# Optimization experiments

Measured on AMD Instinct MI355X. Metric: run time of the kernel, lower is better.

Reference implementation:

```python
import jax, jax.numpy as jnp
import numpy as np

N0, D, H, E0 = 50000, 128, 128, 800000
N1, E1, A, B, C = 20000, 320000, 100000, 64, 10


def _gcn(x, row, col, ew, n, W, b):
    # GCNConv: out = D^-1/2 (A + I) D^-1/2 (x W) + b, with edge weights
    xw = x @ W
    sl = jnp.arange(n)
    r = jnp.concatenate([row, sl])
    c = jnp.concatenate([col, sl])
    w = jnp.concatenate([ew, jnp.ones((n,), ew.dtype)])
    deg = jax.ops.segment_sum(w, c, num_segments=n)
    dinv = jax.lax.rsqrt(jnp.maximum(deg, 1e-12))
    norm = dinv[r] * w * dinv[c]
    return jax.ops.segment_sum(norm[:, None] * xw[r], c, num_segments=n) + b


def _block(x, row, col, ew, n, W1, b1, W2, b2, Wl, bl):
    # Block with num_inner_layers=2, jumping_knowledge='cat'
    x1 = jax.nn.relu(_gcn(x, row, col, ew, n, W1, b1))
    x2 = jax.nn.relu(_gcn(x1, row, col, ew, n, W2, b2))
    return jnp.concatenate([x1, x2], axis=1) @ Wl + bl


def _seg_max(x, idx, n):
    m = jax.ops.segment_max(x, idx, num_segments=n)
    return jnp.where(jnp.isfinite(m), m, 0.0)  # empty segments -> 0 like scatter_max default


def _lin_init(k, i, o):
    s = 1.0 / np.sqrt(i)
    return jax.random.uniform(k, (i, o), jnp.float32, -s, s)


def setup_inputs() -> dict:
    key = jax.random.key(0)
    ks = jax.random.split(key, 20)
    x = jax.random.normal(ks[0], (N0, D), jnp.float32)
    edge_index0 = jax.random.randint(ks[1], (2, E0), 0, N0)
    edge_weight0 = jax.random.uniform(ks[2], (E0,), jnp.float32)
    batch0 = jnp.sort(jax.random.randint(ks[3], (N0,), 0, B))
    cover_row = jax.random.randint(ks[4], (A,), 0, N0)
    cover_col = jnp.concatenate([jnp.arange(N1), jax.random.randint(ks[5], (A - N1,), 0, N1)])
    edge_index1 = jax.random.randint(ks[6], (2, E1), 0, N1)
    edge_weight1 = jax.random.uniform(ks[7], (E1,), jnp.float32)
    batch1 = jnp.sort(jax.random.randint(ks[8], (N1,), 0, B))
    params = dict(
        w_in1=_lin_init(ks[9], D, H), b_in1=jnp.zeros((H,), jnp.float32),
        w_in2=_lin_init(ks[10], H, H), b_in2=jnp.zeros((H,), jnp.float32),
        w_in_lin=_lin_init(ks[11], 2 * H, H), b_in_lin=jnp.zeros((H,), jnp.float32),
        w_b1=_lin_init(ks[12], 2 * H, H), b_b1=jnp.zeros((H,), jnp.float32),
        w_b2=_lin_init(ks[13], H, H), b_b2=jnp.zeros((H,), jnp.float32),
        w_b_lin=_lin_init(ks[14], 2 * H, H), b_b_lin=jnp.zeros((H,), jnp.float32),
        bn_gamma=jnp.ones((4 * H,), jnp.float32), bn_beta=jnp.zeros((4 * H,), jnp.float32),
        w_l1=_lin_init(ks[15], 4 * H, H), b_l1=jnp.zeros((H,), jnp.float32),
        w_l2=_lin_init(ks[16], H, C), b_l2=jnp.zeros((C,), jnp.float32),
    )
    return dict(x=x, edge_index0=edge_index0, edge_weight0=edge_weight0, batch0=batch0,
                cover_row=cover_row, cover_col=cover_col, edge_index1=edge_index1,
                edge_weight1=edge_weight1, batch1=batch1, **params)


def reference(x, edge_index0, edge_weight0, batch0, cover_row, cover_col,
              edge_index1, edge_weight1, batch1,
              w_in1, b_in1, w_in2, b_in2, w_in_lin, b_in_lin,
              w_b1, b_b1, w_b2, b_b2, w_b_lin, b_b_lin,
              bn_gamma, bn_beta, w_l1, b_l1, w_l2, b_l2):
    r0, c0 = edge_index0[0], edge_index0[1]
    h = jax.nn.relu(_block(x, r0, c0, edge_weight0, N0, w_in1, b_in1, w_in2, b_in2, w_in_lin, b_in_lin))
    xs = [jax.ops.segment_sum(h, batch0, num_segments=B), _seg_max(h, batch0, B)]
    # cover_pool_node: add + max over k-plex cover assignments
    hg = h[cover_row]
    h2 = jnp.concatenate([jax.ops.segment_sum(hg, cover_col, num_segments=N1),
                          _seg_max(hg, cover_col, N1)], axis=1)
    r1, c1 = edge_index1[0], edge_index1[1]
    h2 = jax.nn.relu(_block(h2, r1, c1, edge_weight1, N1, w_b1, b_b1, w_b2, b_b2, w_b_lin, b_b_lin))
    xs.append(jax.ops.segment_sum(h2, batch1, num_segments=B))
    xs.append(_seg_max(h2, batch1, B))
    z = jnp.concatenate(xs, axis=1)  # [B, 4H]
    # BatchNorm1d in eval mode: running stats (mean=0, var=1), eps=1e-5
    z = z * (bn_gamma * jax.lax.rsqrt(jnp.asarray(1.0 + 1e-5, z.dtype))) + bn_beta
    z = jax.nn.relu(z @ w_l1 + b_l1)
    logits = z @ w_l2 + b_l2  # dropout skipped (eval mode)
    return jax.nn.softmax(logits, axis=-1)
```

## Files before the change

### kernel.cpp

```cpp
#include <hip/hip_runtime.h>
#include <cmath>

#define HF 128
#define EPB 2048

namespace {

typedef __attribute__((ext_vector_type(8))) short short8;
typedef __attribute__((ext_vector_type(4))) float f32x4;

inline int cdiv(int a, int b) { return (a + b - 1) / b; }

__device__ inline unsigned short f2bf(float x) {
    unsigned u = __float_as_uint(x);
    return (unsigned short)((u + 0x7fffu + ((u >> 16) & 1u)) >> 16);
}
__device__ inline float bf2f(unsigned short u) {
    return __uint_as_float((unsigned)u << 16);
}
__device__ inline float bflo(unsigned v) { return __uint_as_float(v << 16); }
__device__ inline float bfhi(unsigned v) { return __uint_as_float(v & 0xffff0000u); }

#define FIXS 4194304.0f
#define FIXINV 2.384185791015625e-07f
#define SUMMASK ((1ULL << 40) - 1)

template <int K, bool AF32>
__device__ __forceinline__ void gemm_dev(int bid, const void* __restrict__ A1v, int lda1,
                                         const void* __restrict__ A2v, int lda2,
                                         const unsigned short* __restrict__ wpk,
                                         const float* __restrict__ bias, int relu,
                                         unsigned short* __restrict__ out, int N) {
    const int t = threadIdx.x;
    const int wv = t >> 6, lane = t & 63;
    const int l15 = lane & 15, lhi = lane >> 4;
    const int rbase = bid * 128 + wv * 32;

    f32x4 acc[2][8];
#pragma unroll
    for (int i = 0; i < 2; ++i)
#pragma unroll
        for (int g = 0; g < 8; ++g) acc[i][g] = {0.f, 0.f, 0.f, 0.f};

    int r[2];
#pragma unroll
    for (int ri = 0; ri < 2; ++ri) {
        int rr = rbase + ri * 16 + l15;
        r[ri] = (rr < N) ? rr : (N - 1);
    }

    for (int kc = 0; kc < K / 32; ++kc) {
        int kb = kc * 32 + lhi * 8;
        short8 a[2];
#pragma unroll
        for (int ri = 0; ri < 2; ++ri) {
            if (AF32) {
                const float* A = (const float*)A1v;
                const float* p = A + (size_t)r[ri] * lda1 + kb;
                float4 f0 = *reinterpret_cast<const float4*>(p);
                float4 f1 = *reinterpret_cast<const float4*>(p + 4);
                a[ri][0] = (short)f2bf(f0.x); a[ri][1] = (short)f2bf(f0.y);
                a[ri][2] = (short)f2bf(f0.z); a[ri][3] = (short)f2bf(f0.w);
                a[ri][4] = (short)f2bf(f1.x); a[ri][5] = (short)f2bf(f1.y);
                a[ri][6] = (short)f2bf(f1.z); a[ri][7] = (short)f2bf(f1.w);
            } else {
                const unsigned short* base;
                int kk, ld;
                if (K == 256 && kb >= 128) { base = (const unsigned short*)A2v; kk = kb - 128; ld = lda2; }
                else                       { base = (const unsigned short*)A1v; kk = kb;       ld = lda1; }
                a[ri] = *reinterpret_cast<const short8*>(base + (size_t)r[ri] * ld + kk);
            }
        }
        const unsigned short* wb = wpk + (size_t)(kc * 8) * 512 + lane * 8;
#pragma unroll
        for (int g = 0; g < 8; ++g) {
            short8 b = *reinterpret_cast<const short8*>(wb + (size_t)g * 512);
            acc[0][g] = __builtin_amdgcn_mfma_f32_16x16x32_bf16(a[0], b, acc[0][g], 0, 0, 0);
            acc[1][g] = __builtin_amdgcn_mfma_f32_16x16x32_bf16(a[1], b, acc[1][g], 0, 0, 0);
        }
    }

#pragma unroll
    for (int ri = 0; ri < 2; ++ri) {
#pragma unroll
        for (int g = 0; g < 8; ++g) {
            int col = l15 + g * 16;
            float bb = bias ? bias[col] : 0.f;
#pragma unroll
            for (int e = 0; e < 4; ++e) {
                int rr = rbase + ri * 16 + lhi * 4 + e;
                if (rr < N) {
                    float v = acc[ri][g][e] + bb;
                    if (relu) v = fmaxf(v, 0.f);
                    out[(size_t)rr * 128 + col] = f2bf(v);
                }
            }
        }
    }
}

template <int K, bool AF32>
__global__ void k_mfma_gemm(const void* __restrict__ A1v, int lda1,
                            const void* __restrict__ A2v, int lda2,
                            const unsigned short* __restrict__ wpk,
                            const float* __restrict__ bias, int relu,
                            unsigned short* __restrict__ out, int N) {
    gemm_dev<K, AF32>(blockIdx.x, A1v, lda1, A2v, lda2, wpk, bias, relu, out, N);
}

__device__ __forceinline__ void hist_dev(int e, int E, const int* __restrict__ col,
                                         const float* __restrict__ ew,
                                         unsigned long long* __restrict__ dc,
                                         unsigned* __restrict__ rank) {
    if (e < E) {
        unsigned long long v = (1ULL << 40) | (unsigned long long)(ew[e] * FIXS + 0.5f);
        unsigned long long old = atomicAdd(&dc[col[e]], v);
        rank[e] = (unsigned)(old >> 40);
    }
}

__device__ inline void scan256(int* s, int v, int gid, int n, int* __restrict__ excl,
                               int* __restrict__ partial, int pb) {
    s[threadIdx.x] = v;
    __syncthreads();
    for (int off = 1; off < 256; off <<= 1) {
        int t = (threadIdx.x >= off) ? s[threadIdx.x - off] : 0;
        __syncthreads();
        s[threadIdx.x] += t;
        __syncthreads();
    }
    if (gid < n) excl[gid] = s[threadIdx.x] - v;
    if (threadIdx.x == 255) partial[pb] = s[255];
}

__device__ __forceinline__ void fill_dev(int b, int t, const int* __restrict__ row,
                                         const int* __restrict__ col, const float* __restrict__ ew,
                                         const unsigned* __restrict__ rank,
                                         const float* __restrict__ dinv, const int* __restrict__ rp,
                                         int2* __restrict__ ed, int E, int Nn) {
    int xcd = b & 7, chunk = b >> 3;
    int lo = (int)((long long)Nn * xcd >> 3), hi = (int)((long long)Nn * (xcd + 1) >> 3);
    int base = chunk * EPB;
#pragma unroll
    for (int i = 0; i < EPB; i += 256) {
        int e = base + i + t;
        if (e < E) {
            int c = col[e];
            if (c >= lo && c < hi) {
                int r = row[e];
                ed[rp[c] + rank[e]] = make_int2(r, __float_as_int(ew[e] * dinv[r] * dinv[c]));
            }
        }
    }
}

__device__ __forceinline__ void gather_dev(int b, const unsigned* __restrict__ xw, int n,
                                           const int* __restrict__ rp, const int2* __restrict__ ed,
                                           const float* __restrict__ dinv,
                                           const float* __restrict__ bias,
                                           unsigned* __restrict__ out) {
    int wid = (b * 256 + (int)threadIdx.x) >> 6;
    if (wid >= n) return;
    int lane = threadIdx.x & 63;
    int s = rp[wid], e = rp[wid + 1];
    float d = dinv[wid];
    unsigned v = xw[(size_t)wid * 64 + lane];
    float ax = bflo(v) * d * d, ay = bfhi(v) * d * d;
    float bx = 0.f, by = 0.f, cx = 0.f, cy = 0.f, dx = 0.f, dy = 0.f;
    int i = s;
    for (; i + 4 <= e; i += 4) {
        unsigned long long p0 = __builtin_nontemporal_load((const unsigned long long*)(ed + i));
        unsigned long long p1 = __builtin_nontemporal_load((const unsigned long long*)(ed + i + 1));
        unsigned long long p2 = __builtin_nontemporal_load((const unsigned long long*)(ed + i + 2));
        unsigned long long p3 = __builtin_nontemporal_load((const unsigned long long*)(ed + i + 3));
        unsigned v0 = xw[(size_t)(unsigned)(p0 & 0xffffffffu) * 64 + lane];
        unsigned v1 = xw[(size_t)(unsigned)(p1 & 0xffffffffu) * 64 + lane];
        unsigned v2 = xw[(size_t)(unsigned)(p2 & 0xffffffffu) * 64 + lane];
        unsigned v3 = xw[(size_t)(unsigned)(p3 & 0xffffffffu) * 64 + lane];
        float c0 = __uint_as_float((unsigned)(p0 >> 32));
        float c1 = __uint_as_float((unsigned)(p1 >> 32));
        float c2 = __uint_as_float((unsigned)(p2 >> 32));
        float c3 = __uint_as_float((unsigned)(p3 >> 32));
        ax += c0 * bflo(v0); ay += c0 * bfhi(v0);
        bx += c1 * bflo(v1); by += c1 * bfhi(v1);
        cx += c2 * bflo(v2); cy += c2 * bfhi(v2);
        dx += c3 * bflo(v3); dy += c3 * bfhi(v3);
    }
    for (; i < e; ++i) {
        unsigned long long p0 = __builtin_nontemporal_load((const unsigned long long*)(ed + i));
        unsigned v0 = xw[(size_t)(unsigned)(p0 & 0xffffffffu) * 64 + lane];
        float c0 = __uint_as_float((unsigned)(p0 >> 32));
        ax += c0 * bflo(v0); ay += c0 * bfhi(v0);
    }
    ax += bx + cx + dx;
    ay += by + cy + dy;
    float2 bb = *reinterpret_cast<const float2*>(bias + lane * 2);
    ax = fmaxf(ax + bb.x, 0.f);
    ay = fmaxf(ay + bb.y, 0.f);
    out[(size_t)wid * 64 + lane] = (unsigned)f2bf(ax) | ((unsigned)f2bf(ay) << 16);
}

__global__ void k_prep0(const float* __restrict__ w0, const float* __restrict__ w1,
                        const float* __restrict__ w2, const float* __restrict__ w3,
                        const float* __restrict__ w4, const float* __restrict__ w5,
                        unsigned short* __restrict__ wpk,
                        const int* __restrict__ b0, int n0, const int* __restrict__ b1,
                        int n1, int B, int* __restrict__ bst0, int* __restrict__ bst1) {
    int b = blockIdx.x, t = threadIdx.x;
    if (b < 576) {
        int idx = b * 256 + t;
        const float* src; int local;
        if      (idx < 16384)  { src = w0; local = idx; }
        else if (idx < 32768)  { src = w1; local = idx - 16384; }
        else if (idx < 65536)  { src = w2; local = idx - 32768; }
        else if (idx < 98304)  { src = w3; local = idx - 65536; }
        else if (idx < 114688) { src = w4; local = idx - 98304; }
        else                   { src = w5; local = idx - 114688; }
        int e = local & 7, lane = (local >> 3) & 63, g = (local >> 9) & 7, kc = local >> 12;
        int colw = (lane & 15) + 16 * g;
        int k = kc * 32 + ((lane >> 4) << 3) + e;
        wpk[idx] = f2bf(src[k * 128 + colw]);
        return;
    }
    int idx = t;
    if (idx < 2 * (B + 1)) {
        int which = idx > B;
        int bb = which ? idx - (B + 1) : idx;
        const int* arr = which ? b1 : b0;
        int lo = 0, hi = which ? n1 : n0;
        while (lo < hi) {
            int mid = (lo + hi) >> 1;
            if (arr[mid] < bb) lo = mid + 1; else hi = mid;
        }
        (which ? bst1 : bst0)[bb] = lo;
    }
}

__global__ void k_prep1(const float* __restrict__ x, const unsigned short* __restrict__ wpk,
                        unsigned short* __restrict__ xw, int N0gemm, int nbG,
                        const int* __restrict__ col0, const float* __restrict__ ew0,
                        unsigned long long* __restrict__ dc0, unsigned* __restrict__ rank0,
                        int E0) {
    int b = blockIdx.x;
    if (b < nbG) {
        gemm_dev<128, true>(b, x, 128, nullptr, 0, wpk, nullptr, 0, xw, N0gemm);
        return;
    }
    b -= nbG;
    hist_dev(b * 256 + (int)threadIdx.x, E0, col0, ew0, dc0, rank0);
}

__global__ void k_scanA(const unsigned long long* __restrict__ dc0, int* __restrict__ rp0,
                        int* __restrict__ part0, float* __restrict__ dinv0, int n0) {
    __shared__ int s[256];
    int gid = blockIdx.x * 256 + threadIdx.x;
    int v = (gid < n0) ? (int)(dc0[gid] >> 40) : 0;
    scan256(s, v, gid, n0, rp0, part0, blockIdx.x);
    if (gid < n0) dinv0[gid] = rsqrtf(1.0f + (float)(dc0[gid] & SUMMASK) * FIXINV);
}

__global__ void k_scan2a(int* __restrict__ p0, int nb0) {
    __shared__ int s[256];
    int v = (threadIdx.x < nb0) ? p0[threadIdx.x] : 0;
    s[threadIdx.x] = v;
    __syncthreads();
    for (int off = 1; off < 256; off <<= 1) {
        int t = (threadIdx.x >= off) ? s[threadIdx.x - off] : 0;
        __syncthreads();
        s[threadIdx.x] += t;
        __syncthreads();
    }
    if (threadIdx.x < nb0) p0[threadIdx.x] = s[threadIdx.x] - v;
}

__global__ void k_scan3a(int* __restrict__ rp0, const int* __restrict__ part0, int n0, int tot) {
    int gid = blockIdx.x * 256 + threadIdx.x;
    if (gid < n0) rp0[gid] += part0[blockIdx.x];
    if (gid == 0) rp0[n0] = tot;
}

__global__ void k_fill0(const int* __restrict__ row0, const int* __restrict__ col0,
                        const float* __restrict__ ew0, const unsigned* __restrict__ rank0,
                        const float* __restrict__ dinv0, const int* __restrict__ rp0,
                        int2* __restrict__ ed0, int E0, int N0n) {
    fill_dev(blockIdx.x, threadIdx.x, row0, col0, ew0, rank0, dinv0, rp0, ed0, E0, N0n);
}

__global__ void k_gather_hist(const unsigned* __restrict__ xw, int n,
                              const int* __restrict__ rp, const int2* __restrict__ ed,
                              const float* __restrict__ dinv, const float* __restrict__ bias,
                              unsigned* __restrict__ out, int G,
                              const int* __restrict__ col1, const float* __restrict__ ew1,
                              unsigned long long* __restrict__ dc1, unsigned* __restrict__ rank1,
                              int E1, int nb1,
                              const int* __restrict__ ccol, int* __restrict__ ccnt,
                              unsigned* __restrict__ rankc, int A) {
    int b = blockIdx.x;
    if (b < G) { gather_dev(b, xw, n, rp, ed, dinv, bias, out); return; }
    b -= G;
    int t = threadIdx.x;
    if (b < nb1) { hist_dev(b * 256 + t, E1, col1, ew1, dc1, rank1); return; }
    b -= nb1;
    int e = b * 256 + t;
    if (e < A) rankc[e] = (unsigned)atomicAdd(&ccnt[ccol[e]], 1);
}

__global__ void k_gemm_scan(const void* __restrict__ A1v, const unsigned short* __restrict__ wpk,
                            unsigned short* __restrict__ out, int N, int nbG,
                            const unsigned long long* __restrict__ dc1, int* __restrict__ rp1,
                            int* __restrict__ part1, float* __restrict__ dinv1, int n1, int nbs1,
                            const int* __restrict__ ccnt, int* __restrict__ crp,
                            int* __restrict__ cpart, int nc) {
    __shared__ int s[256];
    int b = blockIdx.x;
    if (b < nbG) {
        gemm_dev<128, false>(b, A1v, 128, nullptr, 0, wpk, nullptr, 0, out, N);
        return;
    }
    b -= nbG;
    if (b < nbs1) {
        int gid = b * 256 + threadIdx.x;
        int v = (gid < n1) ? (int)(dc1[gid] >> 40) : 0;
        scan256(s, v, gid, n1, rp1, part1, b);
        if (gid < n1) dinv1[gid] = rsqrtf(1.0f + (float)(dc1[gid] & SUMMASK) * FIXINV);
        return;
    }
    b -= nbs1;
    {
        int gid = b * 256 + threadIdx.x;
        int v = (gid < nc) ? ccnt[gid] : 0;
        scan256(s, v, gid, nc, crp, cpart, b);
    }
}

__global__ void k_scan2b(int* __restrict__ p1, int nb1, int* __restrict__ p2, int nb2) {
    __shared__ int s[256];
    int* p = (blockIdx.x == 0) ? p1 : p2;
    int nb = (blockIdx.x == 0) ? nb1 : nb2;
    int v = (threadIdx.x < nb) ? p[threadIdx.x] : 0;
    s[threadIdx.x] = v;
    __syncthreads();
    for (int off = 1; off < 256; off <<= 1) {
        int t = (threadIdx.x >= off) ? s[threadIdx.x - off] : 0;
        __syncthreads();
        s[threadIdx.x] += t;
        __syncthreads();
    }
    if (threadIdx.x < nb) p[threadIdx.x] = s[threadIdx.x] - v;
}

__global__ void k_scan3b(int* __restrict__ rp1, const int* __restrict__ part1, int n1, int tot1,
                         int nb1, int* __restrict__ crp, const int* __restrict__ cpart,
                         int nc, int totc) {
    int b = blockIdx.x, t = threadIdx.x;
    if (b < nb1) {
        int gid = b * 256 + t;
        if (gid < n1) rp1[gid] += part1[b];
        if (gid == 0) rp1[n1] = tot1;
        return;
    }
    b -= nb1;
    int gid = b * 256 + t;
    if (gid < nc) crp[gid] += cpart[b];
    if (gid == 0) crp[nc] = totc;
}

__global__ void k_gather_fill(const unsigned* __restrict__ xw, int n,
                              const int* __restrict__ rp, const int2* __restrict__ ed,
                              const float* __restrict__ dinv, const float* __restrict__ bias,
                              unsigned* __restrict__ out, int G,
                              const int* __restrict__ row1, const int* __restrict__ col1,
                              const float* __restrict__ ew1, const unsigned* __restrict__ rank1,
                              const float* __restrict__ dinv1, const int* __restrict__ rp1,
                              int2* __restrict__ ed1, int E1, int N1n, int g1b,
                              const int* __restrict__ crow, const int* __restrict__ ccol,
                              const unsigned* __restrict__ rankc, const int* __restrict__ crp,
                              int* __restrict__ csrcs, int A) {
    int b = blockIdx.x, t = threadIdx.x;
    if (b < G) { gather_dev(b, xw, n, rp, ed, dinv, bias, out); return; }
    b -= G;
    if (b < g1b) { fill_dev(b, t, row1, col1, ew1, rank1, dinv1, rp1, ed1, E1, N1n); return; }
    b -= g1b;
    {
        int xcd = b & 7, chunk = b >> 3;
        int lo = (int)((long long)N1n * xcd >> 3), hi = (int)((long long)N1n * (xcd + 1) >> 3);
        int base = chunk * EPB;
#pragma unroll
        for (int i = 0; i < EPB; i += 256) {
            int e = base + i + t;
            if (e < A) {
                int c = ccol[e];
                if (c >= lo && c < hi) csrcs[crp[c] + rankc[e]] = crow[e];
            }
        }
    }
}

__global__ void k_gather(const unsigned* __restrict__ xw, int n, const int* __restrict__ rp,
                         const int2* __restrict__ ed, const float* __restrict__ dinv,
                         const float* __restrict__ bias, unsigned* __restrict__ out) {
    gather_dev(blockIdx.x, xw, n, rp, ed, dinv, bias, out);
}

__global__ void k_pool_cover(const unsigned short* __restrict__ h, const int* __restrict__ bst,
                             float* __restrict__ psum, float* __restrict__ pmax, int nsplit,
                             int nbpool, const unsigned* __restrict__ h32,
                             const int* __restrict__ crp, const int* __restrict__ csrcs,
                             unsigned* __restrict__ h2, int n1) {
    int t = threadIdx.x;
    if ((int)blockIdx.x < nbpool) {
        int blk = blockIdx.x;
        int b = blk / nsplit, sub = (blk % nsplit) * 2 + (t >> 7);
        int col = t & 127;
        int r0 = bst[b], r1 = bst[b + 1];
        float sum = 0.f, mx = 0.f;
        for (int r = r0 + sub; r < r1; r += 2 * nsplit) {
            float v = bf2f(h[(size_t)r * HF + col]);
            sum += v;
            mx = fmaxf(mx, v);
        }
        atomicAdd(&psum[b * HF + col], sum);
        atomicMax(reinterpret_cast<int*>(&pmax[b * HF + col]), __float_as_int(mx));
        return;
    }
    int wid = (((int)blockIdx.x - nbpool) * 256 + t) >> 6;
    if (wid >= n1) return;
    int lane = t & 63;
    int s = crp[wid], e = crp[wid + 1];
    float sx = 0.f, sy = 0.f, mx = 0.f, my = 0.f;
    for (int i = s; i < e; ++i) {
        unsigned v = h32[(size_t)csrcs[i] * 64 + lane];
        float vx = bflo(v), vy = bfhi(v);
        sx += vx; sy += vy;
        mx = fmaxf(mx, vx); my = fmaxf(my, vy);
    }
    h2[(size_t)wid * 128 + lane]      = (unsigned)f2bf(sx) | ((unsigned)f2bf(sy) << 16);
    h2[(size_t)wid * 128 + 64 + lane] = (unsigned)f2bf(mx) | ((unsigned)f2bf(my) << 16);
}

__global__ void k_pool256(const unsigned short* __restrict__ h, const int* __restrict__ bst,
                          float* __restrict__ psum, float* __restrict__ pmax, int nsplit) {
    int t = threadIdx.x;
    int blk = blockIdx.x;
    int b = blk / nsplit, sub = (blk % nsplit) * 2 + (t >> 7);
    int col = t & 127;
    int r0 = bst[b], r1 = bst[b + 1];
    float sum = 0.f, mx = 0.f;
    for (int r = r0 + sub; r < r1; r += 2 * nsplit) {
        float v = bf2f(h[(size_t)r * HF + col]);
        sum += v;
        mx = fmaxf(mx, v);
    }
    atomicAdd(&psum[b * HF + col], sum);
    atomicMax(reinterpret_cast<int*>(&pmax[b * HF + col]), __float_as_int(mx));
}

__global__ void k_head(const float* __restrict__ p0s, const float* __restrict__ p0m,
                       const float* __restrict__ p1s, const float* __restrict__ p1m,
                       const float* __restrict__ gamma, const float* __restrict__ beta,
                       const float* __restrict__ w1, const float* __restrict__ b1,
                       const float* __restrict__ w2, const float* __restrict__ b2,
                       float* __restrict__ out) {
    __shared__ float z[512];
    __shared__ float z1[128];
    __shared__ float lg[10];
    int b = blockIdx.x, t = threadIdx.x;
    const float s = rsqrtf(1.0f + 1e-5f);
    z[t]       = p0s[b * 128 + t] * (gamma[t] * s)       + beta[t];
    z[128 + t] = p0m[b * 128 + t] * (gamma[128 + t] * s) + beta[128 + t];
    z[256 + t] = p1s[b * 128 + t] * (gamma[256 + t] * s) + beta[256 + t];
    z[384 + t] = p1m[b * 128 + t] * (gamma[384 + t] * s) + beta[384 + t];
    __syncthreads();
    float acc = b1[t];
    for (int k = 0; k < 512; ++k) acc += z[k] * w1[k * 128 + t];
    z1[t] = fmaxf(acc, 0.f);
    __syncthreads();
    if (t < 10) {
        float a2 = b2[t];
        for (int k = 0; k < 128; ++k) a2 += z1[k] * w2[k * 10 + t];
        lg[t] = a2;
    }
    __syncthreads();
    if (t == 0) {
        float m = lg[0];
        for (int c = 1; c < 10; ++c) m = fmaxf(m, lg[c]);
        float e[10], ssum = 0.f;
        for (int c = 0; c < 10; ++c) { e[c] = expf(lg[c] - m); ssum += e[c]; }
        for (int c = 0; c < 10; ++c) out[b * 10 + c] = e[c] / ssum;
    }
}

}

extern "C" void kernel_launch(void* const* d_in, const int* in_sizes, int n_in,
                              void* d_out, int out_size, void* d_ws, size_t ws_size,
                              hipStream_t stream) {
    const float* x      = (const float*)d_in[0];
    const int*   ei0    = (const int*)d_in[1];
    const float* ew0    = (const float*)d_in[2];
    const int*   batch0 = (const int*)d_in[3];
    const int*   crow   = (const int*)d_in[4];
    const int*   ccol   = (const int*)d_in[5];
    const int*   ei1    = (const int*)d_in[6];
    const float* ew1    = (const float*)d_in[7];
    const int*   batch1 = (const int*)d_in[8];
    const float* w_in1  = (const float*)d_in[9];
    const float* b_in1  = (const float*)d_in[10];
    const float* w_in2  = (const float*)d_in[11];
    const float* b_in2  = (const float*)d_in[12];
    const float* w_inl  = (const float*)d_in[13];
    const float* b_inl  = (const float*)d_in[14];
    const float* w_b1   = (const float*)d_in[15];
    const float* b_b1   = (const float*)d_in[16];
    const float* w_b2   = (const float*)d_in[17];
    const float* b_b2   = (const float*)d_in[18];
    const float* w_bl   = (const float*)d_in[19];
    const float* b_bl   = (const float*)d_in[20];
    const float* gamma  = (const float*)d_in[21];
    const float* beta   = (const float*)d_in[22];
    const float* w_l1   = (const float*)d_in[23];
    const float* b_l1   = (const float*)d_in[24];
    const float* w_l2   = (const float*)d_in[25];
    const float* b_l2   = (const float*)d_in[26];

    const int N0 = in_sizes[0] / 128;
    const int E0 = in_sizes[2];
    const int A  = in_sizes[4];
    const int E1 = in_sizes[7];
    const int N1 = in_sizes[8];
    const int B  = out_size / 10;

    const int* row0 = ei0;
    const int* col0 = ei0 + E0;
    const int* row1 = ei1;
    const int* col1 = ei1 + E1;

    char* wsp = (char*)d_ws;
    size_t off = 0;
    auto alloc = [&](size_t bytes) -> char* {
        char* p = wsp + off;
        off += (bytes + 255) & ~(size_t)255;
        return p;
    };
    unsigned long long* dc0 = (unsigned long long*)alloc((size_t)N0 * 8);
    unsigned long long* dc1 = (unsigned long long*)alloc((size_t)N1 * 8);
    int*   ccnt  = (int*)alloc((size_t)N1 * 4);
    float* p0s   = (float*)alloc((size_t)B * HF * 4 * 4);
    float* p0m   = p0s + (size_t)B * HF;
    float* p1s   = p0m + (size_t)B * HF;
    float* p1m   = p1s + (size_t)B * HF;
    size_t zero_bytes = off;

    unsigned* xw  = (unsigned*)alloc((size_t)N0 * 64 * 4);
    unsigned* x1  = (unsigned*)alloc((size_t)N0 * 64 * 4);
    unsigned* x2  = (unsigned*)alloc((size_t)N0 * 64 * 4);
    unsigned* h   = (unsigned*)alloc((size_t)N0 * 64 * 4);
    unsigned* h2  = (unsigned*)alloc((size_t)N1 * 128 * 4);
    unsigned short* wpk = (unsigned short*)alloc(147456 * 2);
    float* dinv0 = (float*)alloc((size_t)N0 * 4);
    float* dinv1 = (float*)alloc((size_t)N1 * 4);
    int*   rp0   = (int*)alloc(((size_t)N0 + 1) * 4);
    int*   rp1   = (int*)alloc(((size_t)N1 + 1) * 4);
    int*   crp   = (int*)alloc(((size_t)N1 + 1) * 4);
    int*   part0 = (int*)alloc(256 * 4);
    int*   part1 = (int*)alloc(256 * 4);
    int*   cpart = (int*)alloc(256 * 4);
    int2*  ed0   = (int2*)alloc((size_t)E0 * 8);
    int2*  ed1   = (int2*)alloc((size_t)E1 * 8);
    int*   csrcs = (int*)alloc((size_t)A * 4);
    unsigned* rank0 = (unsigned*)alloc((size_t)E0 * 4);
    unsigned* rank1 = (unsigned*)alloc((size_t)E1 * 4);
    unsigned* rankc = (unsigned*)alloc((size_t)A * 4);
    int*   bst0  = (int*)alloc((size_t)(B + 1) * 4);
    int*   bst1  = (int*)alloc((size_t)(B + 1) * 4);
    (void)ws_size; (void)n_in;

    const int NSPLIT = 16;
    const int nbG0 = cdiv(N0, 128), nbG1 = cdiv(N1, 128);
    const int nbE0 = cdiv(E0, 256), nbE1 = cdiv(E1, 256), nbC = cdiv(A, 256);
    const int nbs0 = cdiv(N0, 256), nbs1 = cdiv(N1, 256), nbsc = cdiv(N1, 256);
    const int g1f = cdiv(E1, EPB) * 8, gcf = cdiv(A, EPB) * 8, g0f = cdiv(E0, EPB) * 8;
    const int G0 = cdiv(N0, 4), G1 = cdiv(N1, 4);

    hipMemsetAsync(dc0, 0, zero_bytes, stream);

    k_prep0<<<577, 256, 0, stream>>>(w_in1, w_in2, w_inl, w_b1, w_b2, w_bl, wpk,
                                     batch0, N0, batch1, N1, B, bst0, bst1);

    k_prep1<<<nbG0 + nbE0, 256, 0, stream>>>(x, wpk, (unsigned short*)xw, N0, nbG0,
                                             col0, ew0, dc0, rank0, E0);

    k_scanA<<<nbs0, 256, 0, stream>>>(dc0, rp0, part0, dinv0, N0);
    k_scan2a<<<1, 256, 0, stream>>>(part0, nbs0);
    k_scan3a<<<nbs0, 256, 0, stream>>>(rp0, part0, N0, E0);
    k_fill0<<<g0f, 256, 0, stream>>>(row0, col0, ew0, rank0, dinv0, rp0, ed0, E0, N0);

    k_gather_hist<<<G0 + nbE1 + nbC, 256, 0, stream>>>(
        xw, N0, rp0, ed0, dinv0, b_in1, x1, G0,
        col1, ew1, dc1, rank1, E1, nbE1, ccol, ccnt, rankc, A);

    k_gemm_scan<<<nbG0 + nbs1 + nbsc, 256, 0, stream>>>(
        x1, wpk + 16384, (unsigned short*)xw, N0, nbG0,
        dc1, rp1, part1, dinv1, N1, nbs1, ccnt, crp, cpart, N1);

    k_scan2b<<<2, 256, 0, stream>>>(part1, nbs1, cpart, nbsc);
    k_scan3b<<<nbs1 + nbsc, 256, 0, stream>>>(rp1, part1, N1, E1, nbs1, crp, cpart, N1, A);

    k_gather_fill<<<G0 + g1f + gcf, 256, 0, stream>>>(
        xw, N0, rp0, ed0, dinv0, b_in2, x2, G0,
        row1, col1, ew1, rank1, dinv1, rp1, ed1, E1, N1, g1f,
        crow, ccol, rankc, crp, csrcs, A);

    k_mfma_gemm<256, false><<<nbG0, 256, 0, stream>>>(
        x1, 128, (const unsigned short*)x2, 128, wpk + 32768, b_inl, 1,
        (unsigned short*)h, N0);

    k_pool_cover<<<B * NSPLIT + cdiv(N1, 4), 256, 0, stream>>>(
        (const unsigned short*)h, bst0, p0s, p0m, NSPLIT, B * NSPLIT,
        h, crp, csrcs, h2, N1);

    k_mfma_gemm<256, false><<<nbG1, 256, 0, stream>>>(
        h2, 256, (const unsigned short*)h2 + 128, 256, wpk + 65536, nullptr, 0,
        (unsigned short*)xw, N1);
    k_gather<<<G1, 256, 0, stream>>>(xw, N1, rp1, ed1, dinv1, b_b1, x1);
    k_mfma_gemm<128, false><<<nbG1, 256, 0, stream>>>(
        x1, 128, nullptr, 0, wpk + 98304, nullptr, 0, (unsigned short*)xw, N1);
    k_gather<<<G1, 256, 0, stream>>>(xw, N1, rp1, ed1, dinv1, b_b2, x2);
    k_mfma_gemm<256, false><<<nbG1, 256, 0, stream>>>(
        x1, 128, (const unsigned short*)x2, 128, wpk + 114688, b_bl, 1,
        (unsigned short*)h, N1);

    k_pool256<<<B * NSPLIT, 256, 0, stream>>>((const unsigned short*)h, bst1, p1s, p1m, NSPLIT);

    k_head<<<B, 128, 0, stream>>>(p0s, p0m, p1s, p1m, gamma, beta, w_l1, b_l1, w_l2, b_l2,
                                  (float*)d_out);
}
```

Measured before the change: 397.6 us.

## Interleave fused kernel roles by block stripes and split gather rows across half-waves

```diff
diff --git a/kernel.cpp b/kernel.cpp
--- a/kernel.cpp
+++ b/kernel.cpp
@@ -8,6 +8,7 @@
 
 typedef __attribute__((ext_vector_type(8))) short short8;
 typedef __attribute__((ext_vector_type(4))) float f32x4;
+typedef unsigned long long u64;
 
 inline int cdiv(int a, int b) { return (a + b - 1) / b; }
 
@@ -24,6 +25,13 @@
 #define FIXS 4194304.0f
 #define FIXINV 2.384185791015625e-07f
 #define SUMMASK ((1ULL << 40) - 1)
+
+__device__ __forceinline__ bool stripeB(int b, int DEN, int& idxA, int& idxB) {
+    int q = b / DEN, r = b - q * DEN;
+    idxB = q;
+    idxA = q * (DEN - 1) + r;
+    return r == DEN - 1;
+}
 
 template <int K, bool AF32>
 __device__ __forceinline__ void gemm_dev(int bid, const void* __restrict__ A1v, int lda1,
@@ -110,11 +118,10 @@
 
 __device__ __forceinline__ void hist_dev(int e, int E, const int* __restrict__ col,
                                          const float* __restrict__ ew,
-                                         unsigned long long* __restrict__ dc,
-                                         unsigned* __restrict__ rank) {
+                                         u64* __restrict__ dc, unsigned* __restrict__ rank) {
     if (e < E) {
-        unsigned long long v = (1ULL << 40) | (unsigned long long)(ew[e] * FIXS + 0.5f);
-        unsigned long long old = atomicAdd(&dc[col[e]], v);
+        u64 v = (1ULL << 40) | (u64)(ew[e] * FIXS + 0.5f);
+        u64 old = atomicAdd(&dc[col[e]], v);
         rank[e] = (unsigned)(old >> 40);
     }
 }
@@ -162,42 +169,111 @@
     int wid = (b * 256 + (int)threadIdx.x) >> 6;
     if (wid >= n) return;
     int lane = threadIdx.x & 63;
+    int half = lane >> 5, l32 = lane & 31;
     int s = rp[wid], e = rp[wid + 1];
-    float d = dinv[wid];
-    unsigned v = xw[(size_t)wid * 64 + lane];
-    float ax = bflo(v) * d * d, ay = bfhi(v) * d * d;
-    float bx = 0.f, by = 0.f, cx = 0.f, cy = 0.f, dx = 0.f, dy = 0.f;
+    f32x4 acc = {0.f, 0.f, 0.f, 0.f};
+    f32x4 acc2 = {0.f, 0.f, 0.f, 0.f};
+    if (half == 0) {
+        float d = dinv[wid];
+        u64 v = *reinterpret_cast<const u64*>(xw + (size_t)wid * 64 + l32 * 2);
+        unsigned w0 = (unsigned)v, w1 = (unsigned)(v >> 32);
+        acc[0] = bflo(w0) * d * d; acc[1] = bfhi(w0) * d * d;
+        acc[2] = bflo(w1) * d * d; acc[3] = bfhi(w1) * d * d;
+    }
     int i = s;
-    for (; i + 4 <= e; i += 4) {
-        unsigned long long p0 = __builtin_nontemporal_load((const unsigned long long*)(ed + i));
-        unsigned long long p1 = __builtin_nontemporal_load((const unsigned long long*)(ed + i + 1));
-        unsigned long long p2 = __builtin_nontemporal_load((const unsigned long long*)(ed + i + 2));
-        unsigned long long p3 = __builtin_nontemporal_load((const unsigned long long*)(ed + i + 3));
-        unsigned v0 = xw[(size_t)(unsigned)(p0 & 0xffffffffu) * 64 + lane];
-        unsigned v1 = xw[(size_t)(unsigned)(p1 & 0xffffffffu) * 64 + lane];
-        unsigned v2 = xw[(size_t)(unsigned)(p2 & 0xffffffffu) * 64 + lane];
-        unsigned v3 = xw[(size_t)(unsigned)(p3 & 0xffffffffu) * 64 + lane];
-        float c0 = __uint_as_float((unsigned)(p0 >> 32));
-        float c1 = __uint_as_float((unsigned)(p1 >> 32));
-        float c2 = __uint_as_float((unsigned)(p2 >> 32));
-        float c3 = __uint_as_float((unsigned)(p3 >> 32));
-        ax += c0 * bflo(v0); ay += c0 * bfhi(v0);
-        bx += c1 * bflo(v1); by += c1 * bfhi(v1);
-        cx += c2 * bflo(v2); cy += c2 * bfhi(v2);
-        dx += c3 * bflo(v3); dy += c3 * bfhi(v3);
-    }
-    for (; i < e; ++i) {
-        unsigned long long p0 = __builtin_nontemporal_load((const unsigned long long*)(ed + i));
-        unsigned v0 = xw[(size_t)(unsigned)(p0 & 0xffffffffu) * 64 + lane];
-        float c0 = __uint_as_float((unsigned)(p0 >> 32));
-        ax += c0 * bflo(v0); ay += c0 * bfhi(v0);
-    }
-    ax += bx + cx + dx;
-    ay += by + cy + dy;
-    float2 bb = *reinterpret_cast<const float2*>(bias + lane * 2);
-    ax = fmaxf(ax + bb.x, 0.f);
-    ay = fmaxf(ay + bb.y, 0.f);
-    out[(size_t)wid * 64 + lane] = (unsigned)f2bf(ax) | ((unsigned)f2bf(ay) << 16);
+    for (; i + 8 <= e; i += 8) {
+        int2 ea = ed[i + half];
+        int2 eb = ed[i + 2 + half];
+        int2 ec = ed[i + 4 + half];
+        int2 eg = ed[i + 6 + half];
+        u64 va = *reinterpret_cast<const u64*>(xw + (size_t)ea.x * 64 + l32 * 2);
+        u64 vb = *reinterpret_cast<const u64*>(xw + (size_t)eb.x * 64 + l32 * 2);
+        u64 vc = *reinterpret_cast<const u64*>(xw + (size_t)ec.x * 64 + l32 * 2);
+        u64 vg = *reinterpret_cast<const u64*>(xw + (size_t)eg.x * 64 + l32 * 2);
+        float ca = __int_as_float(ea.y), cb = __int_as_float(eb.y);
+        float cc = __int_as_float(ec.y), cg = __int_as_float(eg.y);
+        unsigned w;
+        w = (unsigned)va;         acc[0] += ca * bflo(w); acc[1] += ca * bfhi(w);
+        w = (unsigned)(va >> 32); acc[2] += ca * bflo(w); acc[3] += ca * bfhi(w);
+        w = (unsigned)vb;         acc2[0] += cb * bflo(w); acc2[1] += cb * bfhi(w);
+        w = (unsigned)(vb >> 32); acc2[2] += cb * bflo(w); acc2[3] += cb * bfhi(w);
+        w = (unsigned)vc;         acc[0] += cc * bflo(w); acc[1] += cc * bfhi(w);
+        w = (unsigned)(vc >> 32); acc[2] += cc * bflo(w); acc[3] += cc * bfhi(w);
+        w = (unsigned)vg;         acc2[0] += cg * bflo(w); acc2[1] += cg * bfhi(w);
+        w = (unsigned)(vg >> 32); acc2[2] += cg * bflo(w); acc2[3] += cg * bfhi(w);
+    }
+    for (; i + 2 <= e; i += 2) {
+        int2 ea = ed[i + half];
+        u64 va = *reinterpret_cast<const u64*>(xw + (size_t)ea.x * 64 + l32 * 2);
+        float ca = __int_as_float(ea.y);
+        unsigned w;
+        w = (unsigned)va;         acc[0] += ca * bflo(w); acc[1] += ca * bfhi(w);
+        w = (unsigned)(va >> 32); acc[2] += ca * bflo(w); acc[3] += ca * bfhi(w);
+    }
+    if (i < e) {
+        int2 ea = ed[i];
+        u64 va = *reinterpret_cast<const u64*>(xw + (size_t)ea.x * 64 + l32 * 2);
+        float ca = (half == 0) ? __int_as_float(ea.y) : 0.f;
+        unsigned w;
+        w = (unsigned)va;         acc[0] += ca * bflo(w); acc[1] += ca * bfhi(w);
+        w = (unsigned)(va >> 32); acc[2] += ca * bflo(w); acc[3] += ca * bfhi(w);
+    }
+#pragma unroll
+    for (int j = 0; j < 4; ++j) acc[j] += acc2[j];
+#pragma unroll
+    for (int j = 0; j < 4; ++j) acc[j] += __shfl_xor(acc[j], 32, 64);
+    if (half == 0) {
+        float4 bb = *reinterpret_cast<const float4*>(bias + l32 * 4);
+        float r0 = fmaxf(acc[0] + bb.x, 0.f);
+        float r1 = fmaxf(acc[1] + bb.y, 0.f);
+        float r2 = fmaxf(acc[2] + bb.z, 0.f);
+        float r3 = fmaxf(acc[3] + bb.w, 0.f);
+        u64 p = (u64)f2bf(r0) | ((u64)f2bf(r1) << 16) | ((u64)f2bf(r2) << 32) | ((u64)f2bf(r3) << 48);
+        *reinterpret_cast<u64*>(out + (size_t)wid * 64 + l32 * 2) = p;
+    }
+}
+
+__device__ __forceinline__ void cover_dev(int b, const unsigned* __restrict__ h, int n1,
+                                          const int* __restrict__ crp, const int* __restrict__ csrcs,
+                                          unsigned* __restrict__ h2) {
+    int wid = (b * 256 + (int)threadIdx.x) >> 6;
+    if (wid >= n1) return;
+    int lane = threadIdx.x & 63;
+    int half = lane >> 5, l32 = lane & 31;
+    int s = crp[wid], e = crp[wid + 1];
+    f32x4 sm = {0.f, 0.f, 0.f, 0.f};
+    f32x4 mx = {0.f, 0.f, 0.f, 0.f};
+    int i = s;
+    for (; i + 2 <= e; i += 2) {
+        int src = csrcs[i + half];
+        u64 v = *reinterpret_cast<const u64*>(h + (size_t)src * 64 + l32 * 2);
+        unsigned w0 = (unsigned)v, w1 = (unsigned)(v >> 32);
+        float f0 = bflo(w0), f1 = bfhi(w0), f2 = bflo(w1), f3 = bfhi(w1);
+        sm[0] += f0; sm[1] += f1; sm[2] += f2; sm[3] += f3;
+        mx[0] = fmaxf(mx[0], f0); mx[1] = fmaxf(mx[1], f1);
+        mx[2] = fmaxf(mx[2], f2); mx[3] = fmaxf(mx[3], f3);
+    }
+    if (i < e) {
+        int src = csrcs[i];
+        u64 v = *reinterpret_cast<const u64*>(h + (size_t)src * 64 + l32 * 2);
+        unsigned w0 = (unsigned)v, w1 = (unsigned)(v >> 32);
+        float m = (half == 0) ? 1.f : 0.f;
+        float f0 = m * bflo(w0), f1 = m * bfhi(w0), f2 = m * bflo(w1), f3 = m * bfhi(w1);
+        sm[0] += f0; sm[1] += f1; sm[2] += f2; sm[3] += f3;
+        mx[0] = fmaxf(mx[0], f0); mx[1] = fmaxf(mx[1], f1);
+        mx[2] = fmaxf(mx[2], f2); mx[3] = fmaxf(mx[3], f3);
+    }
+#pragma unroll
+    for (int j = 0; j < 4; ++j) {
+        sm[j] += __shfl_xor(sm[j], 32, 64);
+        mx[j] = fmaxf(mx[j], __shfl_xor(mx[j], 32, 64));
+    }
+    if (half == 0) {
+        u64 ps = (u64)f2bf(sm[0]) | ((u64)f2bf(sm[1]) << 16) | ((u64)f2bf(sm[2]) << 32) | ((u64)f2bf(sm[3]) << 48);
+        u64 pm = (u64)f2bf(mx[0]) | ((u64)f2bf(mx[1]) << 16) | ((u64)f2bf(mx[2]) << 32) | ((u64)f2bf(mx[3]) << 48);
+        *reinterpret_cast<u64*>(h2 + (size_t)wid * 128 + l32 * 2) = ps;
+        *reinterpret_cast<u64*>(h2 + (size_t)wid * 128 + 64 + l32 * 2) = pm;
+    }
 }
 
 __global__ void k_prep0(const float* __restrict__ w0, const float* __restrict__ w1,
@@ -205,52 +281,60 @@
                         const float* __restrict__ w4, const float* __restrict__ w5,
                         unsigned short* __restrict__ wpk,
                         const int* __restrict__ b0, int n0, const int* __restrict__ b1,
-                        int n1, int B, int* __restrict__ bst0, int* __restrict__ bst1) {
-    int b = blockIdx.x, t = threadIdx.x;
-    if (b < 576) {
-        int idx = b * 256 + t;
-        const float* src; int local;
-        if      (idx < 16384)  { src = w0; local = idx; }
-        else if (idx < 32768)  { src = w1; local = idx - 16384; }
-        else if (idx < 65536)  { src = w2; local = idx - 32768; }
-        else if (idx < 98304)  { src = w3; local = idx - 65536; }
-        else if (idx < 114688) { src = w4; local = idx - 98304; }
-        else                   { src = w5; local = idx - 114688; }
-        int e = local & 7, lane = (local >> 3) & 63, g = (local >> 9) & 7, kc = local >> 12;
-        int colw = (lane & 15) + 16 * g;
-        int k = kc * 32 + ((lane >> 4) << 3) + e;
-        wpk[idx] = f2bf(src[k * 128 + colw]);
+                        int n1, int B, int* __restrict__ bst0, int* __restrict__ bst1,
+                        const int* __restrict__ col0, const float* __restrict__ ew0,
+                        u64* __restrict__ dc0, unsigned* __restrict__ rank0, int splitE) {
+    int t = threadIdx.x, idxA, idxB;
+    if (stripeB(blockIdx.x, 4, idxA, idxB)) {
+        if (idxB < 576) {
+            int idx = idxB * 256 + t;
+            const float* src; int local;
+            if      (idx < 16384)  { src = w0; local = idx; }
+            else if (idx < 32768)  { src = w1; local = idx - 16384; }
+            else if (idx < 65536)  { src = w2; local = idx - 32768; }
+            else if (idx < 98304)  { src = w3; local = idx - 65536; }
+            else if (idx < 114688) { src = w4; local = idx - 98304; }
+            else                   { src = w5; local = idx - 114688; }
+            int e = local & 7, lane = (local >> 3) & 63, g = (local >> 9) & 7, kc = local >> 12;
+            int colw = (lane & 15) + 16 * g;
+            int k = kc * 32 + ((lane >> 4) << 3) + e;
+            wpk[idx] = f2bf(src[k * 128 + colw]);
+        } else if (idxB == 576) {
+            int idx = t;
+            if (idx < 2 * (B + 1)) {
+                int which = idx > B;
+                int bb = which ? idx - (B + 1) : idx;
+                const int* arr = which ? b1 : b0;
+                int lo = 0, hi = which ? n1 : n0;
+                while (lo < hi) {
+                    int mid = (lo + hi) >> 1;
+                    if (arr[mid] < bb) lo = mid + 1; else hi = mid;
+                }
+                (which ? bst1 : bst0)[bb] = lo;
+            }
+        }
         return;
     }
-    int idx = t;
-    if (idx < 2 * (B + 1)) {
-        int which = idx > B;
-        int bb = which ? idx - (B + 1) : idx;
-        const int* arr = which ? b1 : b0;
-        int lo = 0, hi = which ? n1 : n0;
-        while (lo < hi) {
-            int mid = (lo + hi) >> 1;
-            if (arr[mid] < bb) lo = mid + 1; else hi = mid;
-        }
-        (which ? bst1 : bst0)[bb] = lo;
-    }
+    int e = idxA * 256 + t;
+    if (e < splitE) hist_dev(e, splitE, col0, ew0, dc0, rank0);
 }
 
 __global__ void k_prep1(const float* __restrict__ x, const unsigned short* __restrict__ wpk,
                         unsigned short* __restrict__ xw, int N0gemm, int nbG,
                         const int* __restrict__ col0, const float* __restrict__ ew0,
-                        unsigned long long* __restrict__ dc0, unsigned* __restrict__ rank0,
-                        int E0) {
-    int b = blockIdx.x;
-    if (b < nbG) {
-        gemm_dev<128, true>(b, x, 128, nullptr, 0, wpk, nullptr, 0, xw, N0gemm);
+                        u64* __restrict__ dc0, unsigned* __restrict__ rank0,
+                        int splitE, int E0) {
+    int idxA, idxB;
+    if (stripeB(blockIdx.x, 5, idxA, idxB)) {
+        if (idxB < nbG)
+            gemm_dev<128, true>(idxB, x, 128, nullptr, 0, wpk, nullptr, 0, xw, N0gemm);
         return;
     }
-    b -= nbG;
-    hist_dev(b * 256 + (int)threadIdx.x, E0, col0, ew0, dc0, rank0);
-}
-
-__global__ void k_scanA(const unsigned long long* __restrict__ dc0, int* __restrict__ rp0,
+    int e = splitE + idxA * 256 + (int)threadIdx.x;
+    if (e < E0) hist_dev(e, E0, col0, ew0, dc0, rank0);
+}
+
+__global__ void k_scanA(const u64* __restrict__ dc0, int* __restrict__ rp0,
                         int* __restrict__ part0, float* __restrict__ dinv0, int n0) {
     __shared__ int s[256];
     int gid = blockIdx.x * 256 + threadIdx.x;
@@ -282,55 +366,56 @@
 __global__ void k_fill0(const int* __restrict__ row0, const int* __restrict__ col0,
                         const float* __restrict__ ew0, const unsigned* __restrict__ rank0,
                         const float* __restrict__ dinv0, const int* __restrict__ rp0,
-                        int2* __restrict__ ed0, int E0, int N0n) {
-    fill_dev(blockIdx.x, threadIdx.x, row0, col0, ew0, rank0, dinv0, rp0, ed0, E0, N0n);
-}
-
-__global__ void k_gather_hist(const unsigned* __restrict__ xw, int n,
-                              const int* __restrict__ rp, const int2* __restrict__ ed,
-                              const float* __restrict__ dinv, const float* __restrict__ bias,
-                              unsigned* __restrict__ out, int G,
-                              const int* __restrict__ col1, const float* __restrict__ ew1,
-                              unsigned long long* __restrict__ dc1, unsigned* __restrict__ rank1,
-                              int E1, int nb1,
-                              const int* __restrict__ ccol, int* __restrict__ ccnt,
-                              unsigned* __restrict__ rankc, int A) {
-    int b = blockIdx.x;
-    if (b < G) { gather_dev(b, xw, n, rp, ed, dinv, bias, out); return; }
-    b -= G;
-    int t = threadIdx.x;
-    if (b < nb1) { hist_dev(b * 256 + t, E1, col1, ew1, dc1, rank1); return; }
-    b -= nb1;
-    int e = b * 256 + t;
-    if (e < A) rankc[e] = (unsigned)atomicAdd(&ccnt[ccol[e]], 1);
+                        int2* __restrict__ ed0, int E0, int N0n, int g0f,
+                        const int* __restrict__ col1, const float* __restrict__ ew1,
+                        u64* __restrict__ dc1, unsigned* __restrict__ rank1, int E1, int nbE1,
+                        const int* __restrict__ ccol, int* __restrict__ ccnt,
+                        unsigned* __restrict__ rankc, int A, int nbC) {
+    int t = threadIdx.x, idxA, idxB;
+    if (stripeB(blockIdx.x, 3, idxA, idxB)) {
+        if (idxB < nbE1) { hist_dev(idxB * 256 + t, E1, col1, ew1, dc1, rank1); return; }
+        idxB -= nbE1;
+        if (idxB < nbC) {
+            int e = idxB * 256 + t;
+            if (e < A) rankc[e] = (unsigned)atomicAdd(&ccnt[ccol[e]], 1);
+        }
+        return;
+    }
+    if (idxA < g0f) fill_dev(idxA, t, row0, col0, ew0, rank0, dinv0, rp0, ed0, E0, N0n);
+}
+
+__global__ void k_gather(const unsigned* __restrict__ xw, int n, const int* __restrict__ rp,
+                         const int2* __restrict__ ed, const float* __restrict__ dinv,
+                         const float* __restrict__ bias, unsigned* __restrict__ out) {
+    gather_dev(blockIdx.x, xw, n, rp, ed, dinv, bias, out);
 }
 
 __global__ void k_gemm_scan(const void* __restrict__ A1v, const unsigned short* __restrict__ wpk,
                             unsigned short* __restrict__ out, int N, int nbG,
-                            const unsigned long long* __restrict__ dc1, int* __restrict__ rp1,
+                            const u64* __restrict__ dc1, int* __restrict__ rp1,
                             int* __restrict__ part1, float* __restrict__ dinv1, int n1, int nbs1,
                             const int* __restrict__ ccnt, int* __restrict__ crp,
-                            int* __restrict__ cpart, int nc) {
+                            int* __restrict__ cpart, int nc, int nbsc) {
     __shared__ int s[256];
-    int b = blockIdx.x;
-    if (b < nbG) {
-        gemm_dev<128, false>(b, A1v, 128, nullptr, 0, wpk, nullptr, 0, out, N);
+    int t = threadIdx.x, idxA, idxB;
+    if (stripeB(blockIdx.x, 4, idxA, idxB)) {
+        if (idxB < nbs1) {
+            int gid = idxB * 256 + t;
+            int v = (gid < n1) ? (int)(dc1[gid] >> 40) : 0;
+            scan256(s, v, gid, n1, rp1, part1, idxB);
+            if (gid < n1) dinv1[gid] = rsqrtf(1.0f + (float)(dc1[gid] & SUMMASK) * FIXINV);
+            return;
+        }
+        idxB -= nbs1;
+        if (idxB < nbsc) {
+            int gid = idxB * 256 + t;
+            int v = (gid < nc) ? ccnt[gid] : 0;
+            scan256(s, v, gid, nc, crp, cpart, idxB);
+        }
         return;
     }
-    b -= nbG;
-    if (b < nbs1) {
-        int gid = b * 256 + threadIdx.x;
-        int v = (gid < n1) ? (int)(dc1[gid] >> 40) : 0;
-        scan256(s, v, gid, n1, rp1, part1, b);
-        if (gid < n1) dinv1[gid] = rsqrtf(1.0f + (float)(dc1[gid] & SUMMASK) * FIXINV);
-        return;
-    }
-    b -= nbs1;
-    {
-        int gid = b * 256 + threadIdx.x;
-        int v = (gid < nc) ? ccnt[gid] : 0;
-        scan256(s, v, gid, nc, crp, cpart, b);
-    }
+    if (idxA < nbG)
+        gemm_dev<128, false>(idxA, A1v, 128, nullptr, 0, wpk, nullptr, 0, out, N);
 }
 
 __global__ void k_scan2b(int* __restrict__ p1, int nb1, int* __restrict__ p2, int nb2) {
@@ -375,67 +460,55 @@
                               int2* __restrict__ ed1, int E1, int N1n, int g1b,
                               const int* __restrict__ crow, const int* __restrict__ ccol,
                               const unsigned* __restrict__ rankc, const int* __restrict__ crp,
-                              int* __restrict__ csrcs, int A) {
-    int b = blockIdx.x, t = threadIdx.x;
-    if (b < G) { gather_dev(b, xw, n, rp, ed, dinv, bias, out); return; }
-    b -= G;
-    if (b < g1b) { fill_dev(b, t, row1, col1, ew1, rank1, dinv1, rp1, ed1, E1, N1n); return; }
-    b -= g1b;
-    {
-        int xcd = b & 7, chunk = b >> 3;
-        int lo = (int)((long long)N1n * xcd >> 3), hi = (int)((long long)N1n * (xcd + 1) >> 3);
-        int base = chunk * EPB;
-#pragma unroll
-        for (int i = 0; i < EPB; i += 256) {
-            int e = base + i + t;
-            if (e < A) {
-                int c = ccol[e];
-                if (c >= lo && c < hi) csrcs[crp[c] + rankc[e]] = crow[e];
+                              int* __restrict__ csrcs, int A, int gcb) {
+    int t = threadIdx.x, idxA, idxB;
+    if (stripeB(blockIdx.x, 8, idxA, idxB)) {
+        if (idxB < g1b) {
+            fill_dev(idxB, t, row1, col1, ew1, rank1, dinv1, rp1, ed1, E1, N1n);
+            return;
+        }
+        idxB -= g1b;
+        if (idxB < gcb) {
+            int xcd = idxB & 7, chunk = idxB >> 3;
+            int lo = (int)((long long)N1n * xcd >> 3), hi = (int)((long long)N1n * (xcd + 1) >> 3);
+            int base = chunk * EPB;
+#pragma unroll
+            for (int i = 0; i < EPB; i += 256) {
+                int e = base + i + t;
+                if (e < A) {
+                    int c = ccol[e];
+                    if (c >= lo && c < hi) csrcs[crp[c] + rankc[e]] = crow[e];
+                }
             }
         }
-    }
-}
-
-__global__ void k_gather(const unsigned* __restrict__ xw, int n, const int* __restrict__ rp,
-                         const int2* __restrict__ ed, const float* __restrict__ dinv,
-                         const float* __restrict__ bias, unsigned* __restrict__ out) {
-    gather_dev(blockIdx.x, xw, n, rp, ed, dinv, bias, out);
+        return;
+    }
+    if (idxA < G) gather_dev(idxA, xw, n, rp, ed, dinv, bias, out);
 }
 
 __global__ void k_pool_cover(const unsigned short* __restrict__ h, const int* __restrict__ bst,
                              float* __restrict__ psum, float* __restrict__ pmax, int nsplit,
                              int nbpool, const unsigned* __restrict__ h32,
                              const int* __restrict__ crp, const int* __restrict__ csrcs,
-                             unsigned* __restrict__ h2, int n1) {
-    int t = threadIdx.x;
-    if ((int)blockIdx.x < nbpool) {
-        int blk = blockIdx.x;
-        int b = blk / nsplit, sub = (blk % nsplit) * 2 + (t >> 7);
-        int col = t & 127;
-        int r0 = bst[b], r1 = bst[b + 1];
-        float sum = 0.f, mx = 0.f;
-        for (int r = r0 + sub; r < r1; r += 2 * nsplit) {
-            float v = bf2f(h[(size_t)r * HF + col]);
-            sum += v;
-            mx = fmaxf(mx, v);
-        }
-        atomicAdd(&psum[b * HF + col], sum);
-        atomicMax(reinterpret_cast<int*>(&pmax[b * HF + col]), __float_as_int(mx));
+                             unsigned* __restrict__ h2, int n1, int Gc) {
+    int t = threadIdx.x, idxA, idxB;
+    if (stripeB(blockIdx.x, 6, idxA, idxB)) {
+        if (idxB < nbpool) {
+            int b = idxB / nsplit, sub = (idxB % nsplit) * 2 + (t >> 7);
+            int col = t & 127;
+            int r0 = bst[b], r1 = bst[b + 1];
+            float sum = 0.f, mx = 0.f;
+            for (int r = r0 + sub; r < r1; r += 2 * nsplit) {
+                float v = bf2f(h[(size_t)r * HF + col]);
+                sum += v;
+                mx = fmaxf(mx, v);
+            }
+            atomicAdd(&psum[b * HF + col], sum);
+            atomicMax(reinterpret_cast<int*>(&pmax[b * HF + col]), __float_as_int(mx));
+        }
         return;
     }
-    int wid = (((int)blockIdx.x - nbpool) * 256 + t) >> 6;
-    if (wid >= n1) return;
-    int lane = t & 63;
-    int s = crp[wid], e = crp[wid + 1];
-    float sx = 0.f, sy = 0.f, mx = 0.f, my = 0.f;
-    for (int i = s; i < e; ++i) {
-        unsigned v = h32[(size_t)csrcs[i] * 64 + lane];
-        float vx = bflo(v), vy = bfhi(v);
-        sx += vx; sy += vy;
-        mx = fmaxf(mx, vx); my = fmaxf(my, vy);
-    }
-    h2[(size_t)wid * 128 + lane]      = (unsigned)f2bf(sx) | ((unsigned)f2bf(sy) << 16);
-    h2[(size_t)wid * 128 + 64 + lane] = (unsigned)f2bf(mx) | ((unsigned)f2bf(my) << 16);
+    if (idxA < Gc) cover_dev(idxA, h32, n1, crp, csrcs, h2);
 }
 
 __global__ void k_pool256(const unsigned short* __restrict__ h, const int* __restrict__ bst,
@@ -542,13 +615,13 @@
         off += (bytes + 255) & ~(size_t)255;
         return p;
     };
-    unsigned long long* dc0 = (unsigned long long*)alloc((size_t)N0 * 8);
-    unsigned long long* dc1 = (unsigned long long*)alloc((size_t)N1 * 8);
-    int*   ccnt  = (int*)alloc((size_t)N1 * 4);
-    float* p0s   = (float*)alloc((size_t)B * HF * 4 * 4);
-    float* p0m   = p0s + (size_t)B * HF;
-    float* p1s   = p0m + (size_t)B * HF;
-    float* p1m   = p1s + (size_t)B * HF;
+    u64*  dc0  = (u64*)alloc((size_t)N0 * 8);
+    u64*  dc1  = (u64*)alloc((size_t)N1 * 8);
+    int*  ccnt = (int*)alloc((size_t)N1 * 4);
+    float* p0s = (float*)alloc((size_t)B * HF * 4 * 4);
+    float* p0m = p0s + (size_t)B * HF;
+    float* p1s = p0m + (size_t)B * HF;
+    float* p1m = p1s + (size_t)B * HF;
     size_t zero_bytes = off;
 
     unsigned* xw  = (unsigned*)alloc((size_t)N0 * 64 * 4);
@@ -579,45 +652,68 @@
     const int nbG0 = cdiv(N0, 128), nbG1 = cdiv(N1, 128);
     const int nbE0 = cdiv(E0, 256), nbE1 = cdiv(E1, 256), nbC = cdiv(A, 256);
     const int nbs0 = cdiv(N0, 256), nbs1 = cdiv(N1, 256), nbsc = cdiv(N1, 256);
-    const int g1f = cdiv(E1, EPB) * 8, gcf = cdiv(A, EPB) * 8, g0f = cdiv(E0, EPB) * 8;
+    const int g0f = cdiv(E0, EPB) * 8, g1f = cdiv(E1, EPB) * 8, gcf = cdiv(A, EPB) * 8;
     const int G0 = cdiv(N0, 4), G1 = cdiv(N1, 4);
+    const int histA = (nbE0 + 1) / 2, histB = nbE0 - histA;
+    const int splitE = histA * 256 < E0 ? histA * 256 : E0;
+
+    auto maxi = [](int a, int b) { return a > b ? a : b; };
 
     hipMemsetAsync(dc0, 0, zero_bytes, stream);
 
-    k_prep0<<<577, 256, 0, stream>>>(w_in1, w_in2, w_inl, w_b1, w_b2, w_bl, wpk,
-                                     batch0, N0, batch1, N1, B, bst0, bst1);
-
-    k_prep1<<<nbG0 + nbE0, 256, 0, stream>>>(x, wpk, (unsigned short*)xw, N0, nbG0,
-                                             col0, ew0, dc0, rank0, E0);
+    {
+        int T = 4 * maxi(cdiv(histA, 3), 577);
+        k_prep0<<<T, 256, 0, stream>>>(w_in1, w_in2, w_inl, w_b1, w_b2, w_bl, wpk,
+                                       batch0, N0, batch1, N1, B, bst0, bst1,
+                                       col0, ew0, dc0, rank0, splitE);
+    }
+
+    {
+        int T = 5 * maxi(cdiv(histB, 4), nbG0);
+        k_prep1<<<T, 256, 0, stream>>>(x, wpk, (unsigned short*)xw, N0, nbG0,
+                                       col0, ew0, dc0, rank0, splitE, E0);
+    }
 
     k_scanA<<<nbs0, 256, 0, stream>>>(dc0, rp0, part0, dinv0, N0);
     k_scan2a<<<1, 256, 0, stream>>>(part0, nbs0);
     k_scan3a<<<nbs0, 256, 0, stream>>>(rp0, part0, N0, E0);
-    k_fill0<<<g0f, 256, 0, stream>>>(row0, col0, ew0, rank0, dinv0, rp0, ed0, E0, N0);
-
-    k_gather_hist<<<G0 + nbE1 + nbC, 256, 0, stream>>>(
-        xw, N0, rp0, ed0, dinv0, b_in1, x1, G0,
-        col1, ew1, dc1, rank1, E1, nbE1, ccol, ccnt, rankc, A);
-
-    k_gemm_scan<<<nbG0 + nbs1 + nbsc, 256, 0, stream>>>(
-        x1, wpk + 16384, (unsigned short*)xw, N0, nbG0,
-        dc1, rp1, part1, dinv1, N1, nbs1, ccnt, crp, cpart, N1);
+
+    {
+        int T = 3 * maxi(cdiv(g0f, 2), nbE1 + nbC);
+        k_fill0<<<T, 256, 0, stream>>>(row0, col0, ew0, rank0, dinv0, rp0, ed0, E0, N0, g0f,
+                                       col1, ew1, dc1, rank1, E1, nbE1,
+                                       ccol, ccnt, rankc, A, nbC);
+    }
+
+    k_gather<<<G0, 256, 0, stream>>>(xw, N0, rp0, ed0, dinv0, b_in1, x1);
+
+    {
+        int T = 4 * maxi(cdiv(nbG0, 3), nbs1 + nbsc);
+        k_gemm_scan<<<T, 256, 0, stream>>>(x1, wpk + 16384, (unsigned short*)xw, N0, nbG0,
+                                           dc1, rp1, part1, dinv1, N1, nbs1,
+                                           ccnt, crp, cpart, N1, nbsc);
+    }
 
     k_scan2b<<<2, 256, 0, stream>>>(part1, nbs1, cpart, nbsc);
     k_scan3b<<<nbs1 + nbsc, 256, 0, stream>>>(rp1, part1, N1, E1, nbs1, crp, cpart, N1, A);
 
-    k_gather_fill<<<G0 + g1f + gcf, 256, 0, stream>>>(
-        xw, N0, rp0, ed0, dinv0, b_in2, x2, G0,
-        row1, col1, ew1, rank1, dinv1, rp1, ed1, E1, N1, g1f,
-        crow, ccol, rankc, crp, csrcs, A);
+    {
+        int T = 8 * maxi(cdiv(G0, 7), g1f + gcf);
+        k_gather_fill<<<T, 256, 0, stream>>>(xw, N0, rp0, ed0, dinv0, b_in2, x2, G0,
+                                             row1, col1, ew1, rank1, dinv1, rp1, ed1, E1, N1,
+                                             g1f, crow, ccol, rankc, crp, csrcs, A, gcf);
+    }
 
     k_mfma_gemm<256, false><<<nbG0, 256, 0, stream>>>(
         x1, 128, (const unsigned short*)x2, 128, wpk + 32768, b_inl, 1,
         (unsigned short*)h, N0);
 
-    k_pool_cover<<<B * NSPLIT + cdiv(N1, 4), 256, 0, stream>>>(
-        (const unsigned short*)h, bst0, p0s, p0m, NSPLIT, B * NSPLIT,
-        h, crp, csrcs, h2, N1);
+    {
+        int Gc = cdiv(N1, 4);
+        int T = 6 * maxi(cdiv(Gc, 5), B * NSPLIT);
+        k_pool_cover<<<T, 256, 0, stream>>>((const unsigned short*)h, bst0, p0s, p0m, NSPLIT,
+                                            B * NSPLIT, h, crp, csrcs, h2, N1, Gc);
+    }
 
     k_mfma_gemm<256, false><<<nbG1, 256, 0, stream>>>(
         h2, 256, (const unsigned short*)h2 + 128, 256, wpk + 65536, nullptr, 0,
```

Measured after the change: 383.8 us. 3.5% less time.
